# Performance work log

Hardware: AMD Instinct MI355X
Metric: run time of the kernel (lower is better)

## Reference

```python
import jax, jax.numpy as jnp
import numpy as np

EMB = 384
HEADS = 6
HEAD_SIZE = 64


def setup_inputs() -> dict:
    key = jax.random.key(0)
    ks = jax.random.split(key, 6)
    B, T = 128, 256
    x = jax.random.normal(ks[0], (B, T, EMB), dtype=jnp.float32)
    s = EMB ** -0.5
    Wq = jax.random.normal(ks[1], (HEADS, EMB, HEAD_SIZE), dtype=jnp.float32) * s
    Wk = jax.random.normal(ks[2], (HEADS, EMB, HEAD_SIZE), dtype=jnp.float32) * s
    Wv = jax.random.normal(ks[3], (HEADS, EMB, HEAD_SIZE), dtype=jnp.float32) * s
    Wproj = jax.random.normal(ks[4], (EMB, EMB), dtype=jnp.float32) * s
    bproj = jax.random.normal(ks[5], (EMB,), dtype=jnp.float32) * 0.01
    return {"x": x, "Wq": Wq, "Wk": Wk, "Wv": Wv, "Wproj": Wproj, "bproj": bproj}


def reference(x, Wq, Wk, Wv, Wproj, bproj):
    B, T, C = x.shape
    scale = C ** -0.5  # original scales by embeddingSize**-0.5, not headSize
    q = jnp.einsum('bte,hed->bhtd', x, Wq)
    k = jnp.einsum('bte,hed->bhtd', x, Wk)
    v = jnp.einsum('bte,hed->bhtd', x, Wv)
    w = jnp.einsum('bhtd,bhsd->bhts', q, k) * scale  # (B,H,T,T)
    mask = jnp.tril(jnp.ones((T, T), dtype=bool))
    w = jnp.where(mask[None, None], w, -jnp.inf)
    # original applies softmax over dim=1 of (B,T,T) -> the query axis -> axis=2 here
    w = jax.nn.softmax(w, axis=2)
    out = jnp.einsum('bhts,bhsd->bhtd', w, v)  # (B,H,T,Dh)
    out = out.transpose(0, 2, 1, 3).reshape(B, T, -1)  # concat heads -> (B,T,EMB)
    return out @ Wproj + bproj  # dropout omitted (eval mode)
```

## Files before the change

### kernel.cpp

```cpp
#include <hip/hip_runtime.h>

#define EMB 384
#define HEADS 6
#define DH 64
#define TT 256

constexpr float SCALE = 0.05103103630798288f;

typedef __attribute__((ext_vector_type(8))) short short8;
typedef __attribute__((ext_vector_type(4))) float f32x4;
typedef __attribute__((ext_vector_type(4))) unsigned short u16x4;

__device__ __forceinline__ unsigned short f2bf(float f) {
  unsigned int u = __builtin_bit_cast(unsigned int, f);
  u += 0x7FFFu + ((u >> 16) & 1u);
  return (unsigned short)(u >> 16);
}
__device__ __forceinline__ float bf2f(unsigned short u) {
  unsigned int v = ((unsigned int)u) << 16;
  return __builtin_bit_cast(float, v);
}
__device__ __forceinline__ void gll16(const void* g, void* l) {
  __builtin_amdgcn_global_load_lds(
      (const __attribute__((address_space(1))) unsigned int*)g,
      (__attribute__((address_space(3))) unsigned int*)l, 16, 0, 0);
}

__global__ __launch_bounds__(256)
void cvt_x(const float* __restrict__ x, unsigned short* __restrict__ xb, int n8) {
  int i = blockIdx.x * 256 + threadIdx.x;
  if (i < n8) {
    const float4* src = (const float4*)x;
    float4 a = src[i * 2], b = src[i * 2 + 1];
    short8 o;
    o[0] = (short)f2bf(a.x); o[1] = (short)f2bf(a.y);
    o[2] = (short)f2bf(a.z); o[3] = (short)f2bf(a.w);
    o[4] = (short)f2bf(b.x); o[5] = (short)f2bf(b.y);
    o[6] = (short)f2bf(b.z); o[7] = (short)f2bf(b.w);
    ((short8*)xb)[i] = o;
  }
}

__global__ __launch_bounds__(256)
void build_wt(const float* __restrict__ Wq, const float* __restrict__ Wk,
              const float* __restrict__ Wv, const float* __restrict__ Wp,
              unsigned short* __restrict__ Wt) {
  int idx = blockIdx.x * 256 + threadIdx.x;
  int n = idx / 48, e0 = (idx % 48) * 8;
  const float* src; int stride;
  if (n < 1152) {
    int h = n / 192, rem = n % 192, qkv = rem >> 6, d = rem & 63;
    const float* W = (qkv == 0) ? Wq : (qkv == 1) ? Wk : Wv;
    src = W + ((size_t)h * EMB + e0) * DH + d; stride = DH;
  } else {
    int c = n - 1152;
    src = Wp + (size_t)e0 * EMB + c; stride = EMB;
  }
  short8 o;
  #pragma unroll
  for (int j = 0; j < 8; ++j) o[j] = (short)f2bf(src[j * stride]);
  ((short8*)Wt)[idx] = o;
}

__global__ __launch_bounds__(1024, 1)
void qkv_attn(const unsigned short* __restrict__ xb16, const unsigned short* __restrict__ Wt,
              unsigned short* __restrict__ O)
{
  __shared__ __align__(16) char EL[73728];
  __shared__ __align__(16) char KL[32768];
  __shared__ __align__(16) char VL[32768];
  __shared__ float Lpart[16][256];
  __shared__ float invL[256];

  const int bh = blockIdx.x, tid = (int)threadIdx.x;
  const int w = tid >> 6, lane = tid & 63;
  const int la = lane & 15, kh = lane >> 4;
  const int b = bh / 6, h = bh - b * 6;
  const unsigned short* xb = xb16 + (size_t)b * 256 * 384;
  const unsigned short* Wb = Wt + (size_t)h * 192 * 384;
  char* AL = EL;
  char* BL = EL + 32768;

  const int wr = (w >> 2) * 64, wc = (w & 3) * 48;
  f32x4 acc[4][3];
  #pragma unroll
  for (int i = 0; i < 4; ++i)
    #pragma unroll
    for (int j = 0; j < 3; ++j) acc[i][j] = f32x4{0.f, 0.f, 0.f, 0.f};

  for (int kt = 0; kt < 6; ++kt) {
    if (kt) __syncthreads();
    #pragma unroll
    for (int i = 0; i < 2; ++i) {
      const int Lb = i * 16384 + tid * 16;
      const int row = Lb >> 7;
      const int kcs = ((Lb >> 4) & 7) ^ (row & 7);
      gll16(xb + (size_t)row * 384 + kt * 64 + kcs * 8, AL + Lb);
    }
    {
      const int Lb0 = tid * 16;
      const int row0 = Lb0 >> 7;
      const int kcs0 = ((Lb0 >> 4) & 7) ^ (row0 & 7);
      gll16(Wb + (size_t)row0 * 384 + kt * 64 + kcs0 * 8, BL + Lb0);
      if (tid < 512) {
        const int Lb = 16384 + tid * 16;
        const int row = Lb >> 7;
        const int kcs = ((Lb >> 4) & 7) ^ (row & 7);
        gll16(Wb + (size_t)row * 384 + kt * 64 + kcs * 8, BL + Lb);
      }
    }
    __syncthreads();
    #pragma unroll
    for (int kk = 0; kk < 2; ++kk) {
      const int ch = kk * 4 + kh;
      short8 a[4], bfr[3];
      #pragma unroll
      for (int mi = 0; mi < 4; ++mi) {
        const int r = wr + mi * 16 + la;
        a[mi] = *(const short8*)(AL + r * 128 + ((ch ^ (r & 7)) << 4));
      }
      #pragma unroll
      for (int ni = 0; ni < 3; ++ni) {
        const int rB = wc + ni * 16 + la;
        bfr[ni] = *(const short8*)(BL + rB * 128 + ((ch ^ (rB & 7)) << 4));
      }
      __builtin_amdgcn_s_setprio(1);
      #pragma unroll
      for (int mi = 0; mi < 4; ++mi)
        #pragma unroll
        for (int ni = 0; ni < 3; ++ni)
          acc[mi][ni] = __builtin_amdgcn_mfma_f32_16x16x32_bf16(a[mi], bfr[ni], acc[mi][ni], 0, 0, 0);
      __builtin_amdgcn_s_setprio(0);
    }
  }
  __syncthreads();

  #pragma unroll
  for (int mi = 0; mi < 4; ++mi) {
    #pragma unroll
    for (int ni = 0; ni < 3; ++ni) {
      const int col = wc + ni * 16 + la;
      const int tb = wr + mi * 16 + kh * 4;
      if (col < 64) {
        const int d = col;
        #pragma unroll
        for (int j = 0; j < 4; ++j) {
          const int t = tb + j;
          *(unsigned short*)(EL + t * 128 + (((d >> 3) ^ (t & 7)) << 4) + (d & 7) * 2)
              = f2bf(acc[mi][ni][j]);
        }
      } else if (col < 128) {
        const int d = col - 64;
        #pragma unroll
        for (int j = 0; j < 4; ++j) {
          const int t = tb + j;
          *(unsigned short*)(KL + t * 128 + (((d >> 3) ^ (t & 7)) << 4) + (d & 7) * 2)
              = f2bf(acc[mi][ni][j]);
        }
      } else {
        const int d = col - 128;
        u16x4 pk;
        #pragma unroll
        for (int j = 0; j < 4; ++j) pk[j] = f2bf(acc[mi][ni][j]);
        *(u16x4*)(VL + d * 512 + (((tb >> 3) ^ (d & 7)) << 4) + (tb & 7) * 2) = pk;
      }
    }
  }
  __syncthreads();

  const int p = w >> 1;
  const int rts[2] = { p, 15 - p };
  short8 qa[2][2];
  #pragma unroll
  for (int ti = 0; ti < 2; ++ti)
    #pragma unroll
    for (int kk = 0; kk < 2; ++kk) {
      const int r = rts[ti] * 16 + la;
      const int ch = kk * 4 + kh;
      qa[ti][kk] = *(const short8*)(EL + r * 128 + ((ch ^ (r & 7)) << 4));
    }
  __syncthreads();

  int wps[2], eoffs[2];
  #pragma unroll
  for (int ti = 0; ti < 2; ++ti) {
    const int rt = rts[ti];
    wps[ti] = 32 * ((rt + 2) >> 1);
    const int S = (rt & 1) ? ((rt + 1) * (rt + 1) / 4) : (rt * (rt + 2) / 4);
    eoffs[ti] = 1024 * S;
  }

  #pragma unroll
  for (int i = 0; i < 4; ++i) Lpart[w][i * 64 + lane] = 0.f;

  #pragma unroll
  for (int ti = 0; ti < 2; ++ti) {
    const int rt = rts[ti], wp = wps[ti], stride = wp * 2;
    char* Ebase = EL + eoffs[ti];
    const int nns = wp >> 4;
    for (int ns = (w & 1); ns < nns; ns += 2) {
      f32x4 s4 = f32x4{0.f, 0.f, 0.f, 0.f};
      #pragma unroll
      for (int kk = 0; kk < 2; ++kk) {
        const int rB = ns * 16 + la, kc = kk * 4 + kh;
        short8 bf = *(const short8*)(KL + rB * 128 + ((kc ^ (rB & 7)) << 4));
        s4 = __builtin_amdgcn_mfma_f32_16x16x32_bf16(qa[ti][kk], bf, s4, 0, 0, 0);
      }
      const int c = ns * 16 + la, cc = c >> 3, co = (c & 7) * 2;
      float ps = 0.f;
      #pragma unroll
      for (int j = 0; j < 4; ++j) {
        const int r = kh * 4 + j;
        const int t = rt * 16 + r;
        const float e = (t >= c) ? __expf(s4[j] * SCALE) : 0.f;
        ps += e;
        *(unsigned short*)(Ebase + r * stride + ((cc ^ (r & 3)) << 4) + co) = f2bf(e);
      }
      ps += __shfl_xor(ps, 16);
      ps += __shfl_xor(ps, 32);
      if (kh == 0) Lpart[w][c] += ps;
    }
  }
  __syncthreads();

  if (tid < 256) {
    float Ls = 0.f;
    #pragma unroll
    for (int ww = 0; ww < 16; ++ww) Ls += Lpart[ww][tid];
    invL[tid] = 1.f / Ls;
  }
  __syncthreads();

  {
    const int d = tid >> 4, qq = tid & 15;
    #pragma unroll
    for (int i = 0; i < 2; ++i) {
      const int kcp = qq * 2 + i;
      char* pch = VL + d * 512 + kcp * 16;
      short8 v = *(short8*)pch;
      const int sb = (kcp ^ (d & 7)) * 8;
      short8 o;
      #pragma unroll
      for (int e = 0; e < 8; ++e)
        o[e] = (short)f2bf(bf2f((unsigned short)v[e]) * invL[sb + e]);
      *(short8*)pch = o;
    }
  }
  __syncthreads();

  unsigned short* Og = O + (size_t)b * 256 * 384 + h * 64;
  {
    const int ti = (w & 1) ? 0 : 1;
    const int rt = rts[ti], wp = wps[ti], stride = wp * 2;
    const char* Ebase = EL + eoffs[ti];
    f32x4 oacc[4];
    #pragma unroll
    for (int nd = 0; nd < 4; ++nd) oacc[nd] = f32x4{0.f, 0.f, 0.f, 0.f};
    const int nks = wp >> 5;
    for (int ks = 0; ks < nks; ++ks) {
      const int cc = ks * 4 + kh;
      short8 ea = *(const short8*)(Ebase + la * stride + ((cc ^ (la & 3)) << 4));
      __builtin_amdgcn_s_setprio(1);
      #pragma unroll
      for (int nd = 0; nd < 4; ++nd) {
        const int d = nd * 16 + la;
        short8 vb = *(const short8*)(VL + d * 512 + ((cc ^ (d & 7)) << 4));
        oacc[nd] = __builtin_amdgcn_mfma_f32_16x16x32_bf16(ea, vb, oacc[nd], 0, 0, 0);
      }
      __builtin_amdgcn_s_setprio(0);
    }
    #pragma unroll
    for (int nd = 0; nd < 4; ++nd) {
      const int d = nd * 16 + la;
      #pragma unroll
      for (int j = 0; j < 4; ++j) {
        const int t = rt * 16 + kh * 4 + j;
        Og[(size_t)t * 384 + d] = f2bf(oacc[nd][j]);
      }
    }
  }
}

__global__ __launch_bounds__(512, 1)
void proj_gemm(const unsigned short* __restrict__ A, const unsigned short* __restrict__ Bt,
               float* __restrict__ Co, const float* __restrict__ bias)
{
  __shared__ __align__(16) unsigned short AL[128 * 384];
  __shared__ __align__(16) unsigned short BL[2][128 * 64];
  const int tid = (int)threadIdx.x, w = tid >> 6, lane = tid & 63;
  const int la = lane & 15, kh = lane >> 4;
  const int m0 = blockIdx.x * 128;

  {
    const int row = tid >> 2, qq = tid & 3;
    const short8* O8 = (const short8*)(A + (size_t)(m0 + row) * 384);
    #pragma unroll
    for (int i = 0; i < 12; ++i) {
      const int ch = qq + 4 * i;
      *(short8*)((char*)AL + row * 768 + ((ch ^ (row & 7)) << 4)) = O8[ch];
    }
  }

  auto stageB = [&](int buf, int n0, int k0) {
    #pragma unroll
    for (int i = 0; i < 2; ++i) {
      const int Lb = i * 8192 + tid * 16;
      const int row = Lb >> 7;
      const int kcs = ((Lb >> 4) & 7) ^ (row & 7);
      gll16(Bt + (size_t)(n0 + row) * 384 + k0 + kcs * 8, (char*)BL[buf] + Lb);
    }
  };

  stageB(0, 0, 0);
  __syncthreads();

  const int wr = (w >> 2) * 64, wc = (w & 3) * 32;
  int buf = 0;
  for (int nt = 0; nt < 3; ++nt) {
    f32x4 acc[4][2];
    #pragma unroll
    for (int i = 0; i < 4; ++i) { acc[i][0] = f32x4{0.f,0.f,0.f,0.f}; acc[i][1] = f32x4{0.f,0.f,0.f,0.f}; }

    for (int kt = 0; kt < 6; ++kt) {
      if (kt < 5)          stageB(buf ^ 1, nt * 128, (kt + 1) * 64);
      else if (nt + 1 < 3) stageB(buf ^ 1, (nt + 1) * 128, 0);
      #pragma unroll
      for (int kk = 0; kk < 2; ++kk) {
        short8 a[4], bb[2];
        const int chA = kt * 8 + kk * 4 + kh;
        #pragma unroll
        for (int mi = 0; mi < 4; ++mi) {
          const int r = wr + mi * 16 + la;
          a[mi] = *(const short8*)((const char*)AL + r * 768 + ((chA ^ (r & 7)) << 4));
        }
        const int chB = kk * 4 + kh;
        #pragma unroll
        for (int ni = 0; ni < 2; ++ni) {
          const int rB = wc + ni * 16 + la;
          bb[ni] = *(const short8*)((const char*)BL[buf] + rB * 128 + ((chB ^ (rB & 7)) << 4));
        }
        __builtin_amdgcn_s_setprio(1);
        #pragma unroll
        for (int mi = 0; mi < 4; ++mi)
          #pragma unroll
          for (int ni = 0; ni < 2; ++ni)
            acc[mi][ni] = __builtin_amdgcn_mfma_f32_16x16x32_bf16(a[mi], bb[ni], acc[mi][ni], 0, 0, 0);
        __builtin_amdgcn_s_setprio(0);
      }
      __syncthreads();
      buf ^= 1;
    }

    #pragma unroll
    for (int mi = 0; mi < 4; ++mi) {
      const int mbase = m0 + wr + mi * 16 + kh * 4;
      #pragma unroll
      for (int ni = 0; ni < 2; ++ni) {
        const int nl = nt * 128 + wc + ni * 16 + la;
        const float bn = bias[nl];
        #pragma unroll
        for (int j = 0; j < 4; ++j)
          Co[(size_t)(mbase + j) * 384 + nl] = acc[mi][ni][j] + bn;
      }
    }
  }
}

__global__ __launch_bounds__(256, 1)
void mha_fused(const float* __restrict__ x, const float* __restrict__ Wq,
               const float* __restrict__ Wk, const float* __restrict__ Wv,
               const float* __restrict__ Wp, const float* __restrict__ bp,
               float* __restrict__ out)
{
  const int bh = blockIdx.x;
  const int b = bh / HEADS, h = bh % HEADS;
  const int tid = (int)threadIdx.x;
  const int wave = tid >> 6, lane = tid & 63;
  const float* xb = x + (size_t)b * TT * EMB;
  const float* wq = Wq + (size_t)h * EMB * DH;
  const float* wk = Wk + (size_t)h * EMB * DH;
  const float* wv = Wv + (size_t)h * EMB * DH;
  __shared__ float Ks[TT][68];
  __shared__ float Vs[TT][64];
  __shared__ float Qt[64][68];
  for (int c = 0; c < 4; ++c) {
    const int s0 = wave * 64 + c * 16;
    float ak[16], av[16];
    #pragma unroll
    for (int r = 0; r < 16; ++r) { ak[r] = 0.f; av[r] = 0.f; }
    for (int e = 0; e < EMB; ++e) {
      const float kk = wk[e * DH + lane];
      const float vv = wv[e * DH + lane];
      #pragma unroll
      for (int r = 0; r < 16; ++r) {
        const float xv = xb[(s0 + r) * EMB + e];
        ak[r] += xv * kk; av[r] += xv * vv;
      }
    }
    #pragma unroll
    for (int r = 0; r < 16; ++r) { Ks[s0 + r][lane] = ak[r]; Vs[s0 + r][lane] = av[r]; }
  }
  __syncthreads();
  const int s = tid;
  float kreg[64];
  {
    const float4* k4 = (const float4*)&Ks[s][0];
    #pragma unroll
    for (int i = 0; i < 16; ++i) {
      float4 kv = k4[i];
      kreg[4*i+0] = kv.x; kreg[4*i+1] = kv.y; kreg[4*i+2] = kv.z; kreg[4*i+3] = kv.w;
    }
  }
  float Lsum = 0.f;
  for (int tile = 0; tile < 4; ++tile) {
    {
      const int r0 = tile * 64 + wave * 16;
      float aq[16];
      #pragma unroll
      for (int r = 0; r < 16; ++r) aq[r] = 0.f;
      for (int e = 0; e < EMB; ++e) {
        const float qw = wq[e * DH + lane];
        #pragma unroll
        for (int r = 0; r < 16; ++r) aq[r] += xb[(r0 + r) * EMB + e] * qw;
      }
      __syncthreads();
      #pragma unroll
      for (int r = 0; r < 16; ++r) Qt[wave*16 + r][lane] = aq[r];
      __syncthreads();
    }
    const int tbase = tile * 64;
    if (tbase + 63 >= s) {
      for (int tr = 0; tr < 64; ++tr) {
        const int t = tbase + tr;
        if (t < s) continue;
        float w = 0.f;
        const float4* q4 = (const float4*)&Qt[tr][0];
        #pragma unroll
        for (int i = 0; i < 16; ++i) {
          float4 qv = q4[i];
          w += qv.x*kreg[4*i+0] + qv.y*kreg[4*i+1] + qv.z*kreg[4*i+2] + qv.w*kreg[4*i+3];
        }
        Lsum += __expf(w * SCALE);
      }
    }
  }
  __syncthreads();
  {
    const float invL = 1.0f / Lsum;
    float4* v4 = (float4*)&Vs[s][0];
    #pragma unroll
    for (int i = 0; i < 16; ++i) {
      float4 vv = v4[i];
      vv.x *= invL; vv.y *= invL; vv.z *= invL; vv.w *= invL;
      v4[i] = vv;
    }
  }
  __syncthreads();
  const float bias1 = bp[tid];
  const float bias2 = (tid < 128) ? bp[256 + tid] : 0.f;
  const int tr = tid >> 2, dq = tid & 3;
  float* ob = out + (size_t)b * TT * EMB;
  for (int tile = 0; tile < 4; ++tile) {
    {
      const int r0 = tile * 64 + wave * 16;
      float aq[16];
      #pragma unroll
      for (int r = 0; r < 16; ++r) aq[r] = 0.f;
      for (int e = 0; e < EMB; ++e) {
        const float qw = wq[e * DH + lane];
        #pragma unroll
        for (int r = 0; r < 16; ++r) aq[r] += xb[(r0 + r) * EMB + e] * qw;
      }
      __syncthreads();
      #pragma unroll
      for (int r = 0; r < 16; ++r) Qt[wave*16 + r][lane] = aq[r];
      __syncthreads();
    }
    const int t = tile * 64 + tr;
    float qreg[16];
    {
      const float4* q4 = (const float4*)&Qt[tr][dq * 16];
      #pragma unroll
      for (int i = 0; i < 4; ++i) {
        float4 qv = q4[i];
        qreg[4*i+0] = qv.x; qreg[4*i+1] = qv.y; qreg[4*i+2] = qv.z; qreg[4*i+3] = qv.w;
      }
    }
    float acc[16];
    #pragma unroll
    for (int i = 0; i < 16; ++i) acc[i] = 0.f;
    for (int s2 = 0; s2 <= t; ++s2) {
      const float4* kk4 = (const float4*)&Ks[s2][dq * 16];
      float part = 0.f;
      #pragma unroll
      for (int i = 0; i < 4; ++i) {
        float4 kv = kk4[i];
        part += qreg[4*i+0]*kv.x + qreg[4*i+1]*kv.y + qreg[4*i+2]*kv.z + qreg[4*i+3]*kv.w;
      }
      part += __shfl_xor(part, 1);
      part += __shfl_xor(part, 2);
      const float p = __expf(part * SCALE);
      const float4* vv4 = (const float4*)&Vs[s2][dq * 16];
      #pragma unroll
      for (int i = 0; i < 4; ++i) {
        float4 vv = vv4[i];
        acc[4*i+0] += p * vv.x; acc[4*i+1] += p * vv.y;
        acc[4*i+2] += p * vv.z; acc[4*i+3] += p * vv.w;
      }
    }
    __syncthreads();
    #pragma unroll
    for (int i = 0; i < 16; ++i) Qt[tr][dq*16 + i] = acc[i];
    __syncthreads();
    const int c1 = tid;
    const int c2 = 256 + tid;
    for (int rg = 0; rg < 4; ++rg) {
      float a1[16], a2[16];
      #pragma unroll
      for (int r = 0; r < 16; ++r) { a1[r] = 0.f; a2[r] = 0.f; }
      for (int d = 0; d < 64; ++d) {
        const float wp1 = Wp[(size_t)(h*64 + d) * EMB + c1];
        const float wp2 = (tid < 128) ? Wp[(size_t)(h*64 + d) * EMB + c2] : 0.f;
        #pragma unroll
        for (int r = 0; r < 16; ++r) {
          const float a = Qt[rg*16 + r][d];
          a1[r] += a * wp1; a2[r] += a * wp2;
        }
      }
      if (h == 0) {
        #pragma unroll
        for (int r = 0; r < 16; ++r) { a1[r] += bias1; a2[r] += bias2; }
      }
      const int trow0 = tile*64 + rg*16;
      #pragma unroll
      for (int r = 0; r < 16; ++r)
        atomicAdd(&ob[(size_t)(trow0 + r) * EMB + c1], a1[r]);
      if (tid < 128) {
        #pragma unroll
        for (int r = 0; r < 16; ++r)
          atomicAdd(&ob[(size_t)(trow0 + r) * EMB + c2], a2[r]);
      }
    }
    __syncthreads();
  }
}

extern "C" void kernel_launch(void* const* d_in, const int* in_sizes, int n_in,
                              void* d_out, int out_size, void* d_ws, size_t ws_size,
                              hipStream_t stream) {
  const float* x  = (const float*)d_in[0];
  const float* Wq = (const float*)d_in[1];
  const float* Wk = (const float*)d_in[2];
  const float* Wv = (const float*)d_in[3];
  const float* Wp = (const float*)d_in[4];
  const float* bp = (const float*)d_in[5];

  const int nb = in_sizes[0] / (TT * EMB);
  const size_t M = (size_t)nb * TT;
  const size_t XB = M * EMB * 2;
  const size_t WT = (size_t)1536 * 384 * 2;

  const size_t off_x  = 0;
  const size_t off_wt = XB;
  const size_t off_o  = off_wt + WT;
  const size_t need   = off_o + XB;

  if (ws_size < need) {
    hipMemsetAsync(d_out, 0, (size_t)out_size * sizeof(float), stream);
    mha_fused<<<nb * HEADS, 256, 0, stream>>>(x, Wq, Wk, Wv, Wp, bp, (float*)d_out);
    return;
  }

  char* ws = (char*)d_ws;
  unsigned short* xb16 = (unsigned short*)(ws + off_x);
  unsigned short* Wt   = (unsigned short*)(ws + off_wt);
  unsigned short* Ow   = (unsigned short*)(ws + off_o);

  const int n8 = (int)(M * EMB / 8);
  cvt_x<<<(n8 + 255) / 256, 256, 0, stream>>>(x, xb16, n8);
  build_wt<<<288, 256, 0, stream>>>(Wq, Wk, Wv, Wp, Wt);

  qkv_attn<<<nb * HEADS, 1024, 0, stream>>>(xb16, Wt, Ow);

  proj_gemm<<<(unsigned)(M / 128), 512, 0, stream>>>(
      Ow, Wt + (size_t)1152 * 384, (float*)d_out, bp);
}
```

Measured before the change: 117.0 us.

## Double-buffer QKV GEMM loads and remap blocks for L2 locality

New measurement: 106.2 us. 1.1x faster.

```diff
diff --git a/kernel.cpp b/kernel.cpp
--- a/kernel.cpp
+++ b/kernel.cpp
@@ -72,14 +72,17 @@
   __shared__ float Lpart[16][256];
   __shared__ float invL[256];
 
-  const int bh = blockIdx.x, tid = (int)threadIdx.x;
+  const int bhRaw = blockIdx.x, tid = (int)threadIdx.x;
+  const int bh = (bhRaw & 7) * 96 + (bhRaw >> 3);
   const int w = tid >> 6, lane = tid & 63;
   const int la = lane & 15, kh = lane >> 4;
   const int b = bh / 6, h = bh - b * 6;
   const unsigned short* xb = xb16 + (size_t)b * 256 * 384;
   const unsigned short* Wb = Wt + (size_t)h * 192 * 384;
-  char* AL = EL;
-  char* BL = EL + 32768;
+  char* A0 = EL;
+  char* B0 = EL + 32768;
+  char* A1 = KL;
+  char* B1 = VL;
 
   const int wr = (w >> 2) * 64, wc = (w & 3) * 48;
   f32x4 acc[4][3];
@@ -88,28 +91,29 @@
     #pragma unroll
     for (int j = 0; j < 3; ++j) acc[i][j] = f32x4{0.f, 0.f, 0.f, 0.f};
 
-  for (int kt = 0; kt < 6; ++kt) {
-    if (kt) __syncthreads();
+  auto stage = [&](char* A, char* B, int kt) {
     #pragma unroll
     for (int i = 0; i < 2; ++i) {
       const int Lb = i * 16384 + tid * 16;
       const int row = Lb >> 7;
       const int kcs = ((Lb >> 4) & 7) ^ (row & 7);
-      gll16(xb + (size_t)row * 384 + kt * 64 + kcs * 8, AL + Lb);
+      gll16(xb + (size_t)row * 384 + kt * 64 + kcs * 8, A + Lb);
     }
     {
       const int Lb0 = tid * 16;
       const int row0 = Lb0 >> 7;
       const int kcs0 = ((Lb0 >> 4) & 7) ^ (row0 & 7);
-      gll16(Wb + (size_t)row0 * 384 + kt * 64 + kcs0 * 8, BL + Lb0);
+      gll16(Wb + (size_t)row0 * 384 + kt * 64 + kcs0 * 8, B + Lb0);
       if (tid < 512) {
         const int Lb = 16384 + tid * 16;
         const int row = Lb >> 7;
         const int kcs = ((Lb >> 4) & 7) ^ (row & 7);
-        gll16(Wb + (size_t)row * 384 + kt * 64 + kcs * 8, BL + Lb);
-      }
-    }
-    __syncthreads();
+        gll16(Wb + (size_t)row * 384 + kt * 64 + kcs * 8, B + Lb);
+      }
+    }
+  };
+
+  auto compute = [&](const char* A, const char* B) {
     #pragma unroll
     for (int kk = 0; kk < 2; ++kk) {
       const int ch = kk * 4 + kh;
@@ -117,12 +121,12 @@
       #pragma unroll
       for (int mi = 0; mi < 4; ++mi) {
         const int r = wr + mi * 16 + la;
-        a[mi] = *(const short8*)(AL + r * 128 + ((ch ^ (r & 7)) << 4));
+        a[mi] = *(const short8*)(A + r * 128 + ((ch ^ (r & 7)) << 4));
       }
       #pragma unroll
       for (int ni = 0; ni < 3; ++ni) {
         const int rB = wc + ni * 16 + la;
-        bfr[ni] = *(const short8*)(BL + rB * 128 + ((ch ^ (rB & 7)) << 4));
+        bfr[ni] = *(const short8*)(B + rB * 128 + ((ch ^ (rB & 7)) << 4));
       }
       __builtin_amdgcn_s_setprio(1);
       #pragma unroll
@@ -132,8 +136,20 @@
           acc[mi][ni] = __builtin_amdgcn_mfma_f32_16x16x32_bf16(a[mi], bfr[ni], acc[mi][ni], 0, 0, 0);
       __builtin_amdgcn_s_setprio(0);
     }
-  }
-  __syncthreads();
+  };
+
+  stage(A0, B0, 0);
+  __syncthreads();
+  #pragma unroll
+  for (int g = 0; g < 3; ++g) {
+    const int k1 = 2 * g + 1;
+    stage(A1, B1, k1);
+    compute(A0, B0);
+    __syncthreads();
+    if (k1 + 1 < 6) stage(A0, B0, k1 + 1);
+    compute(A1, B1);
+    __syncthreads();
+  }
 
   #pragma unroll
   for (int mi = 0; mi < 4; ++mi) {
@@ -565,7 +581,7 @@
   const size_t off_o  = off_wt + WT;
   const size_t need   = off_o + XB;
 
-  if (ws_size < need) {
+  if (ws_size < need || nb * HEADS != 768) {
     hipMemsetAsync(d_out, 0, (size_t)out_size * sizeof(float), stream);
     mha_fused<<<nb * HEADS, 256, 0, stream>>>(x, Wq, Wk, Wv, Wp, bp, (float*)d_out);
     return;
```
